# Kernel tuning notes

Hardware: AMD Instinct MI355X
Metric: run time of the kernel (lower is better)

Reference implementation:

```python
import jax, jax.numpy as jnp
import numpy as np
from jax import lax

RATE = 2
KSIZE = 3
FUSE_K = 3
SOFTMAX_SCALE = 10.0
EPS = 1e-8


def extract_patches(x, k, s):
    """ZeroPad2d(1) then unfold: x [B,C,H,W] -> patches [B, oh*ow, C, k, k]."""
    xp = jnp.pad(x, ((0, 0), (0, 0), (1, 1), (1, 1)))
    B, C, Hp, Wp = xp.shape
    oh = (Hp - k) // s + 1
    ow = (Wp - k) // s + 1
    ii = (jnp.arange(oh) * s)[:, None] + jnp.arange(k)[None, :]   # [oh,k]
    jj = (jnp.arange(ow) * s)[:, None] + jnp.arange(k)[None, :]   # [ow,k]
    p = xp[:, :, ii[:, :, None, None], jj[None, None, :, :]]      # [B,C,oh,k,ow,k]
    p = p.transpose(0, 2, 4, 1, 3, 5).reshape(B, oh * ow, C, k, k)
    return p


def _fuse_conv(a, eye):
    # a: [B,1,N,M]; 3x3 identity-diagonal smoothing conv, padding 1
    return lax.conv_general_dilated(a, eye, (1, 1), [(1, 1), (1, 1)],
                                    dimension_numbers=('NCHW', 'OIHW', 'NCHW'))


def contextual_attention(in_data, mask):
    B, C, H, W = in_data.shape
    Cf = C // 2
    f_full = in_data[:, :Cf]          # narrow(1,0,C//2)
    b_full = in_data[:, :Cf]          # source narrows the SAME slice for b
    mask_f = mask.astype(in_data.dtype)
    rate = RATE
    kernel = 2 * rate

    # raw 4x4 patches of full-res background (deconv filters), [B,L,Cf,4,4]
    raw_w = extract_patches(b_full, kernel, rate)

    # nearest downsample by 1/rate == strided slicing
    f = f_full[:, :, ::rate, ::rate]
    b = b_full[:, :, ::rate, ::rate]
    h, w = f.shape[2], f.shape[3]
    L = h * w

    # 3x3 matching patches of downsampled background, L2-normalized per patch
    wpat = extract_patches(b, KSIZE, 1)                              # [B,L,Cf,3,3]
    norm = jnp.sqrt(jnp.sum(wpat * wpat, axis=(2, 3, 4), keepdims=True))
    wn = wpat / jnp.maximum(norm, EPS)

    # per-sample conv2d(xi, wi_normed, padding=1) == patch/patch correlation
    fp = extract_patches(f, KSIZE, 1)                                # [B,hw,Cf,3,3]
    yi = jnp.einsum('bpckl,bqckl->bqp', fp, wn).reshape(B, L, h, w)  # [B,L,h,w]

    # fuse: two diagonal 3x3 smoothing passes over the [L, h*w] score matrix
    eye = jnp.eye(FUSE_K, dtype=in_data.dtype).reshape(1, 1, FUSE_K, FUSE_K)
    A = yi.reshape(B, 1, L, h * w)
    A = _fuse_conv(A, eye)
    A = A.reshape(B, h, w, h, w).transpose(0, 2, 1, 4, 3).reshape(B, 1, w * h, w * h)
    A = _fuse_conv(A, eye)
    A = A.reshape(B, w, h, w, h).transpose(0, 2, 1, 4, 3)
    yi = A.reshape(B, L, h, w)

    # mask gate: mm = 1 where the 3x3 mask patch is all-zero
    mpat = extract_patches(mask_f, KSIZE, 1)[0]                      # [L,1,3,3]
    m_mean = jnp.mean(mpat, axis=(1, 2, 3))                          # [L]
    mm = (m_mean == 0.0).astype(in_data.dtype)[None, :, None, None]
    yi = yi * mm
    yi = jax.nn.softmax(yi * SOFTMAX_SCALE, axis=1)
    yi = yi * mm

    # conv_transpose2d(yi, raw_wi, stride=rate, padding=1) / 4 per sample
    def agg(y1, rw):
        rhs = jnp.flip(rw, (-2, -1)).transpose(1, 0, 2, 3)           # [Cf,L,4,4]
        return lax.conv_general_dilated(y1[None], rhs, (1, 1), [(2, 2), (2, 2)],
                                        lhs_dilation=(rate, rate),
                                        dimension_numbers=('NCHW', 'OIHW', 'NCHW'))[0]
    y = jax.vmap(agg)(yi, raw_w) / 4.0                               # [B,Cf,H,W]

    # masked_fill_(inv_mask, 0) == multiply by {0,1} mask, upsampled to H x W
    mask_up = jnp.repeat(jnp.repeat(mask_f, rate, axis=2), rate, axis=3)
    y = y * mask_up

    return jnp.concatenate([b_full, f_full, y], axis=1)             # [B,3*Cf,H,W]


def setup_inputs() -> dict:
    key = jax.random.key(0)
    k1, k2 = jax.random.split(key)
    in_data = jax.random.normal(k1, (2, 128, 128, 128), dtype=jnp.float32)
    mask = jax.random.randint(k2, (1, 1, 64, 64), 0, 2, dtype=jnp.int32)
    return {"in_data": in_data, "mask": mask}


def reference(in_data, mask):
    return contextual_attention(in_data, mask)
```

## Files before the change

kernel.cpp:

```cpp
#include <hip/hip_runtime.h>
#include <math.h>

#define MAX_SLOTS 64
#define L 4096

#define OFF_CNT   0
#define OFF_LIST  64
#define OFF_FSUB  512
#define OFF_K5    2230784
#define OFF_SF    4065792

__device__ __forceinline__ void build_list(const int* __restrict__ mask,
                                           unsigned int* flagw, int* llist,
                                           int* lcnt) {
    int tid = threadIdx.x;
    for (int w = tid; w < 128; w += 256) flagw[w] = 0u;
    __syncthreads();
    int q0 = tid * 16;
    unsigned int mybits = 0u;
    for (int k = 0; k < 16; ++k) {
        int q = q0 + k;
        int qi = q >> 6, qj = q & 63;
        bool allz = true;
        for (int dy = -1; dy <= 1; ++dy)
            for (int dx = -1; dx <= 1; ++dx) {
                int y = qi + dy, x = qj + dx;
                if (y >= 0 && y < 64 && x >= 0 && x < 64)
                    allz = allz && (mask[y * 64 + x] == 0);
            }
        if (allz) mybits |= (1u << k);
    }
    if (mybits) atomicOr(&flagw[q0 >> 5], mybits << (q0 & 31));
    __syncthreads();
    if (tid < 64) {
        unsigned int w0 = flagw[2 * tid], w1 = flagw[2 * tid + 1];
        int own = __popc(w0) + __popc(w1);
        int inc = own;
        for (int o = 1; o < 64; o <<= 1) {
            int v = __shfl_up(inc, o);
            if (tid >= o) inc += v;
        }
        int pos = inc - own;
        for (int k = 0; k < 32; ++k)
            if (w0 & (1u << k)) { if (pos < MAX_SLOTS) llist[pos] = tid * 64 + k; ++pos; }
        for (int k = 0; k < 32; ++k)
            if (w1 & (1u << k)) { if (pos < MAX_SLOTS) llist[pos] = tid * 64 + 32 + k; ++pos; }
        if (tid == 63) *lcnt = (inc < MAX_SLOTS) ? inc : MAX_SLOTS;
    }
    __syncthreads();
}

__global__ __launch_bounds__(256) void k_front(const float* __restrict__ in,
                                               const int* __restrict__ mask,
                                               int* __restrict__ cnt,
                                               int* __restrict__ list,
                                               float* __restrict__ fsub,
                                               float* __restrict__ K5,
                                               float* __restrict__ sf,
                                               float* __restrict__ out) {
    __shared__ float patch9[5184];
    __shared__ unsigned int flagw[128];
    __shared__ int llist[MAX_SLOTS];
    __shared__ int lcnt;
    __shared__ int iflags[16];
    int tid = threadIdx.x;
    int blk = blockIdx.x;

    if (blk < 128) {
        int slot = blk & 63, b = blk >> 6;
        build_list(mask, flagw, llist, &lcnt);
        int nact = lcnt;
        if (blk == 0) {
            if (tid < MAX_SLOTS) list[tid] = llist[tid];
            if (tid == 64) *cnt = nact;
        }
        if (slot >= nact) {
            for (int t = tid; t < 1600; t += 256) {
                int c = t / 25, e = t - c * 25;
                K5[(((size_t)b * 64 + c) * 64 + slot) * 28 + e] = 0.f;
            }
            return;
        }
        if (tid < 16) iflags[tid] = 0;
        __syncthreads();
        int Q = llist[slot];
        const float* inb = in + (size_t)b * 2097152;
        int w = tid >> 6, lane = tid & 63;
        for (int combo = w; combo < 9; combo += 4) {
            int d2 = combo / 3 - 1, d1 = combo % 3 - 1;
            int XQ = ((Q & 63) << 6) + (Q >> 6) + d2;
            if (XQ < 0 || XQ >= L) continue;
            int YQ = ((XQ & 63) << 6) + (XQ >> 6);
            int R = YQ + d1;
            if (R < 0 || R >= L) continue;
            if (lane == 0) iflags[combo] = 1;
            int ri = R >> 6, rj = R & 63;
            float vals[9]; float ss = 0.f;
            #pragma unroll
            for (int k = 0; k < 9; ++k) {
                int t = lane + (k << 6);
                int c = t / 9; int tap = t - c * 9;
                int dy = tap / 3, dx = tap - dy * 3;
                int yy = ri + dy - 1, xx = rj + dx - 1;
                float v = ((unsigned)yy < 64u && (unsigned)xx < 64u)
                          ? inb[((size_t)c << 14) + (yy << 8) + (xx << 1)] : 0.f;
                vals[k] = v; ss += v * v;
            }
            for (int o = 32; o > 0; o >>= 1) ss += __shfl_xor(ss, o);
            float inv = 1.f / fmaxf(sqrtf(ss), 1e-8f);
            float* dst = patch9 + combo * 576;
            #pragma unroll
            for (int k = 0; k < 9; ++k) dst[lane + (k << 6)] = vals[k] * inv;
        }
        __syncthreads();
        for (int t = tid; t < 1600; t += 256) {
            int c = t / 25, e = t - c * 25;
            int oy = e / 5 - 2, ox = e - (e / 5) * 5 - 2;
            float s = 0.f;
            for (int dy = -1; dy <= 1; ++dy) {
                int dd2 = oy - dy; if (dd2 < -1 || dd2 > 1) continue;
                for (int dx = -1; dx <= 1; ++dx) {
                    int dd1 = ox - dx; if (dd1 < -1 || dd1 > 1) continue;
                    int combo = (dd2 + 1) * 3 + (dd1 + 1);
                    if (iflags[combo])
                        s += patch9[combo * 576 + c * 9 + (dy + 1) * 3 + (dx + 1)];
                }
            }
            K5[(((size_t)b * 64 + c) * 64 + slot) * 28 + e] = s;
        }
        return;
    }

    int idx = (blk - 128) * 256 + tid;
    int j = idx & 63;
    int i = (idx >> 6) & 63;
    int c = (idx >> 12) & 63;
    int b = idx >> 18;
    float v = in[(((b * 128 + c) * 128) + 2 * i) * 128 + 2 * j];
    fsub[(size_t)b * 278784 + c * 4356 + (i + 1) * 66 + (j + 1)] = v;
    sf[idx] = 0.f;
    if (idx < 33280) {
        int plane = idx / 260;
        int r = idx - plane * 260;
        int pb = plane >> 6, pc = plane & 63;
        int row, col;
        if (r < 66) { row = 0; col = r; }
        else if (r < 132) { row = 65; col = r - 66; }
        else { int rr = r - 132; row = (rr >> 1) + 1; col = (rr & 1) ? 65 : 0; }
        fsub[(size_t)pb * 278784 + pc * 4356 + row * 66 + col] = 0.f;
    }
    #pragma unroll
    for (int k = 0; k < 4; ++k) {
        int t = idx + k * 524288;
        int pix = t & 16383;
        int cc = (t >> 14) & 63;
        int bb = t >> 20;
        float pv = in[(size_t)(bb * 128 + cc) * 16384 + pix];
        size_t ob = (size_t)bb * 3145728;
        out[ob + (size_t)cc * 16384 + pix] = pv;
        out[ob + (size_t)(cc + 64) * 16384 + pix] = pv;
    }
}

__global__ __launch_bounds__(256) void k_mid2(const int* __restrict__ cnt,
                                              const int* __restrict__ list,
                                              const float* __restrict__ fsub,
                                              const float* __restrict__ K5,
                                              float* __restrict__ sf) {
    __shared__ float smem[840];
    int tid = threadIdx.x;
    int blk = blockIdx.x;
    int nact = min(*cnt, MAX_SLOTS);
    if (nact == 0) return;

    if (blk < 496) {
        int wid = __builtin_amdgcn_readfirstlane(blk * 4 + (tid >> 6));
        int j = tid & 63;
        int r   = 1 + (wid % 62);
        int cg2 = (wid / 62) & 15;
        int b   = wid / 992;
        int jc = min(max(j, 1), 62);
        const float* F = fsub + (size_t)b * 278784;
        int base = (r - 1) * 66 + (jc - 1);
        bool active = (j >= 1 && j <= 62);
        int P = (r << 6) + j;
        for (int s0 = 0; s0 < nact; s0 += 16) {
            float acc[16];
            #pragma unroll
            for (int s = 0; s < 16; ++s) acc[s] = 0.f;
            #pragma unroll
            for (int cc = 0; cc < 4; ++cc) {
                int c = cg2 * 4 + cc;
                const float* Fc = F + c * 4356 + base;
                float win[25];
                #pragma unroll
                for (int dy = 0; dy < 5; ++dy)
                    #pragma unroll
                    for (int dx = 0; dx < 5; ++dx)
                        win[dy * 5 + dx] = Fc[dy * 66 + dx];
                const float* kc = K5 + (((size_t)b * 64 + c) * 64 + s0) * 28;
                #pragma unroll
                for (int s = 0; s < 16; ++s) {
                    #pragma unroll
                    for (int k = 0; k < 25; ++k)
                        acc[s] += kc[s * 28 + k] * win[k];
                }
            }
            if (active) {
                int smax = min(16, nact - s0);
                for (int s = 0; s < smax; ++s)
                    atomicAdd(&sf[((size_t)b * 64 + (s0 + s)) * 4096 + P], acc[s]);
            }
        }
        return;
    }

    int bt = blk - 496;
    int combo = bt % 9; int rest = bt / 9;
    int slot = rest & 63, b = rest >> 6;
    if (slot >= nact) return;
    int d2 = combo / 3 - 1, d1 = combo % 3 - 1;
    int Q = list[slot];
    int XQ = ((Q & 63) << 6) + (Q >> 6) + d2;
    if (XQ < 0 || XQ >= L) return;
    int YQ = ((XQ & 63) << 6) + (XQ >> 6);
    int R = YQ + d1;
    if (R < 0 || R >= L) return;
    int ri = R >> 6, rj = R & 63;
    const float* F = fsub + (size_t)b * 278784;
    float* patch = smem;
    float* red = smem + 576;
    const float* Fp = F + ri * 66 + rj;
    auto ld = [&](int t) -> float {
        int c = t / 9; int tap = t - c * 9;
        int dy = tap / 3, dx = tap - dy * 3;
        return Fp[c * 4356 + dy * 66 + dx];
    };
    float v0 = ld(tid), v1 = ld(tid + 256), v2 = (tid < 64) ? ld(tid + 512) : 0.f;
    red[tid] = v0 * v0 + v1 * v1 + v2 * v2;
    __syncthreads();
    if (tid < 64) {
        float a = red[tid] + red[tid + 64] + red[tid + 128] + red[tid + 192];
        for (int o = 32; o > 0; o >>= 1) a += __shfl_xor(a, o);
        if (tid == 0) smem[832] = 1.f / fmaxf(sqrtf(a), 1e-8f);
    }
    __syncthreads();
    float inv = smem[832];
    patch[tid] = v0 * inv; patch[tid + 256] = v1 * inv;
    if (tid < 64) patch[tid + 512] = v2 * inv;
    __syncthreads();
    if (tid >= 252) return;
    int i, j;
    if (tid < 64)       { i = 0;  j = tid; }
    else if (tid < 128) { i = 63; j = tid - 64; }
    else if (tid < 190) { i = tid - 127; j = 0; }
    else                { i = tid - 189; j = 63; }
    int P = (i << 6) + j;
    int XP = (j << 6) + i + d2;
    if (XP < 0 || XP >= L) return;
    int YP = ((XP & 63) << 6) + (XP >> 6);
    int Z = YP + d1;
    if (Z < 0 || Z >= L) return;
    int pi = Z >> 6, pj = Z & 63;
    const float* Fz = F + pi * 66 + pj;
    float dot = 0.f;
    #pragma unroll 4
    for (int c = 0; c < 64; ++c) {
        const float* Fc = Fz + c * 4356;
        const float* pc = patch + c * 9;
        dot += Fc[0] * pc[0]   + Fc[1] * pc[1]   + Fc[2] * pc[2];
        dot += Fc[66] * pc[3]  + Fc[67] * pc[4]  + Fc[68] * pc[5];
        dot += Fc[132] * pc[6] + Fc[133] * pc[7] + Fc[134] * pc[8];
    }
    atomicAdd(&sf[((size_t)b * 64 + slot) * 4096 + P], dot);
}

__global__ __launch_bounds__(256) void k_tail2(const float* __restrict__ in,
                                               const int* __restrict__ mask,
                                               const int* __restrict__ cnt,
                                               const int* __restrict__ list,
                                               const float* __restrict__ sf,
                                               float* __restrict__ out) {
    __shared__ float sw16[16 * 192];
    __shared__ float pat16[16 * 128];
    __shared__ float Mv[192];
    __shared__ float Dv[192];
    int tid = threadIdx.x;
    int nact = min(*cnt, MAX_SLOTS);
    int up = blockIdx.x, cg8 = blockIdx.y, b = blockIdx.z;
    int c0 = cg8 * 8;
    const float* inb0 = in + (size_t)b * 2097152 + (size_t)c0 * 16384;
    const float* sfb = sf + (size_t)b * 262144;

    if (tid < 192) {
        int i = up - 1 + (tid >> 6); int jj = tid & 63;
        float M = 0.f, invden = 0.f;
        if ((unsigned)i < 64u && nact > 0) {
            const float* sp = sfb + (i << 6) + jj;
            for (int s = 0; s < nact; ++s)
                M = fmaxf(M, 10.f * sp[(size_t)s * 4096]);
            float den = (float)(L - nact) * expf(-M);
            for (int s = 0; s < nact; ++s)
                den += expf(10.f * sp[(size_t)s * 4096] - M);
            invden = 1.f / den;
        }
        Mv[tid] = M; Dv[tid] = invden;
    }

    int uu = tid >> 7, v = tid & 127;
    int u = up * 2 + uu;
    bool gate = (mask[(u >> 1) * 64 + (v >> 1)] != 0) && (nact > 0);
    int Wp[4]; int tap[4]; bool val[4];
    {
        int pa = (u + 1) & 1, pb_ = (v + 1) & 1;
        int i0 = (u + 1 - pa) >> 1, j0 = (v + 1 - pb_) >> 1;
        #pragma unroll
        for (int di = 0; di < 2; ++di)
            #pragma unroll
            for (int dj = 0; dj < 2; ++dj) {
                int p = di * 2 + dj;
                int ii = i0 - di, jx = j0 - dj;
                int iis = ii - (up - 1);
                val[p] = (jx >= 0 && jx < 64);
                Wp[p] = val[p] ? (iis * 64 + jx) : 0;
                tap[p] = (pa + 2 * di) * 4 + (pb_ + 2 * dj);
            }
    }
    float y[8];
    #pragma unroll
    for (int cc = 0; cc < 8; ++cc) y[cc] = 0.f;

    for (int s0 = 0; s0 < nact; s0 += 16) {
        int ns = min(16, nact - s0);
        __syncthreads();
        for (int t = tid; t < ns * 192; t += 256) {
            int sl = t / 192; int rr = t - sl * 192;
            int i = up - 1 + (rr >> 6); int jj = rr & 63;
            float wv = 0.f;
            if ((unsigned)i < 64u)
                wv = expf(10.f * sfb[(size_t)(s0 + sl) * 4096 + (i << 6) + jj] - Mv[rr]) * Dv[rr];
            sw16[t] = wv;
        }
        for (int t = tid; t < ns * 128; t += 256) {
            int sl = t >> 7; int rr = t & 127;
            int cc = rr >> 4; int e = rr & 15; int aa = e >> 2; int bb = e & 3;
            int q = list[s0 + sl]; int qi = q >> 6, qj = q & 63;
            int row = 2 * qi - 1 + aa, col = 2 * qj - 1 + bb;
            float pv = (row >= 0 && row < 128 && col >= 0 && col < 128)
                       ? inb0[(size_t)cc * 16384 + row * 128 + col] : 0.f;
            pat16[t] = pv;
        }
        __syncthreads();
        if (gate) {
            for (int s = 0; s < ns; ++s) {
                const float* wrow = sw16 + s * 192;
                const float* ps = pat16 + s * 128;
                #pragma unroll
                for (int p = 0; p < 4; ++p) {
                    if (!val[p]) continue;
                    float wv = wrow[Wp[p]];
                    #pragma unroll
                    for (int cc = 0; cc < 8; ++cc)
                        y[cc] += wv * ps[cc * 16 + tap[p]];
                }
            }
        }
    }
    if (gate) {
        #pragma unroll
        for (int cc = 0; cc < 8; ++cc) y[cc] *= 0.25f;
    }
    size_t ob = (size_t)b * 3145728 + (size_t)(c0 + 128) * 16384 + (size_t)u * 128 + v;
    #pragma unroll
    for (int cc = 0; cc < 8; ++cc)
        out[ob + (size_t)cc * 16384] = y[cc];
}

extern "C" void kernel_launch(void* const* d_in, const int* in_sizes, int n_in,
                              void* d_out, int out_size, void* d_ws, size_t ws_size,
                              hipStream_t stream) {
    const float* in = (const float*)d_in[0];
    const int* mask = (const int*)d_in[1];
    float* out = (float*)d_out;
    char* ws = (char*)d_ws;
    int* cnt    = (int*)(ws + OFF_CNT);
    int* list   = (int*)(ws + OFF_LIST);
    float* fsub = (float*)(ws + OFF_FSUB);
    float* K5   = (float*)(ws + OFF_K5);
    float* sf   = (float*)(ws + OFF_SF);

    k_front<<<2176, 256, 0, stream>>>(in, mask, cnt, list, fsub, K5, sf, out);
    k_mid2<<<1648, 256, 0, stream>>>(cnt, list, fsub, K5, sf);
    k_tail2<<<dim3(64, 8, 2), 256, 0, stream>>>(in, mask, cnt, list, sf, out);
}
```

Baseline: 146.0 us.

## Fuse three kernels into one persistent kernel with grid-wide barriers

Merges the front, mid and tail kernels into a single persistent kernel of 1024 blocks that loops over the old block indices and separates the phases with a software global barrier built on atomics. The aim is to remove two kernel launches and the gaps between them. It also vectorizes the copy to the output and the zeroing of sf with float4, and cuts the slot batch in the mid phase from 16 to 8 to save registers. In exchange it relies on all 1024 blocks being resident at once (launch bounds 256,4), pays for spin-wait barriers, and every phase now shares one pool of shared memory.

Measured after the change: 513.5 us. 3.52x slower.

```diff
diff --git a/kernel.cpp b/kernel.cpp
--- a/kernel.cpp
+++ b/kernel.cpp
@@ -3,12 +3,35 @@
 
 #define MAX_SLOTS 64
 #define L 4096
+#define NBLK 1024
 
 #define OFF_CNT   0
 #define OFF_LIST  64
 #define OFF_FSUB  512
 #define OFF_K5    2230784
 #define OFF_SF    4065792
+
+__device__ unsigned int g_bar[4];
+
+__device__ __forceinline__ void global_barrier(int which) {
+    __syncthreads();
+    if (threadIdx.x == 0) {
+        unsigned int* cntp = &g_bar[which * 2];
+        unsigned int* genp = &g_bar[which * 2 + 1];
+        __threadfence();
+        unsigned int g = __hip_atomic_load(genp, __ATOMIC_RELAXED, __HIP_MEMORY_SCOPE_AGENT);
+        unsigned int a = __hip_atomic_fetch_add(cntp, 1u, __ATOMIC_ACQ_REL, __HIP_MEMORY_SCOPE_AGENT);
+        if (a == gridDim.x - 1) {
+            __hip_atomic_store(cntp, 0u, __ATOMIC_RELAXED, __HIP_MEMORY_SCOPE_AGENT);
+            __hip_atomic_store(genp, g + 1u, __ATOMIC_RELEASE, __HIP_MEMORY_SCOPE_AGENT);
+        } else {
+            while (__hip_atomic_load(genp, __ATOMIC_RELAXED, __HIP_MEMORY_SCOPE_AGENT) == g)
+                __builtin_amdgcn_s_sleep(1);
+        }
+        __threadfence();
+    }
+    __syncthreads();
+}
 
 __device__ __forceinline__ void build_list(const int* __restrict__ mask,
                                            unsigned int* flagw, int* llist,
@@ -50,330 +73,335 @@
     __syncthreads();
 }
 
-__global__ __launch_bounds__(256) void k_front(const float* __restrict__ in,
-                                               const int* __restrict__ mask,
-                                               int* __restrict__ cnt,
-                                               int* __restrict__ list,
-                                               float* __restrict__ fsub,
-                                               float* __restrict__ K5,
-                                               float* __restrict__ sf,
-                                               float* __restrict__ out) {
-    __shared__ float patch9[5184];
+__global__ __launch_bounds__(256, 4) void k_all(const float* __restrict__ in,
+                                                const int* __restrict__ mask,
+                                                int* __restrict__ cnt,
+                                                int* __restrict__ list,
+                                                float* __restrict__ fsub,
+                                                float* __restrict__ K5,
+                                                float* __restrict__ sf,
+                                                float* __restrict__ out) {
+    __shared__ float pool[5504];
     __shared__ unsigned int flagw[128];
     __shared__ int llist[MAX_SLOTS];
     __shared__ int lcnt;
     __shared__ int iflags[16];
     int tid = threadIdx.x;
-    int blk = blockIdx.x;
-
-    if (blk < 128) {
-        int slot = blk & 63, b = blk >> 6;
-        build_list(mask, flagw, llist, &lcnt);
-        int nact = lcnt;
-        if (blk == 0) {
-            if (tid < MAX_SLOTS) list[tid] = llist[tid];
-            if (tid == 64) *cnt = nact;
-        }
-        if (slot >= nact) {
-            for (int t = tid; t < 1600; t += 256) {
-                int c = t / 25, e = t - c * 25;
-                K5[(((size_t)b * 64 + c) * 64 + slot) * 28 + e] = 0.f;
-            }
-            return;
-        }
-        if (tid < 16) iflags[tid] = 0;
+    int bid = blockIdx.x;
+
+    for (int tt = bid; tt < 2176; tt += NBLK) {
+        if (tt < 128) {
+            int slot = tt & 63, b = tt >> 6;
+            build_list(mask, flagw, llist, &lcnt);
+            int nact = lcnt;
+            if (tt == 0) {
+                if (tid < MAX_SLOTS) list[tid] = llist[tid];
+                if (tid == 64) *cnt = nact;
+            }
+            if (slot >= nact) {
+                for (int t = tid; t < 1600; t += 256) {
+                    int c = t / 25, e = t - c * 25;
+                    K5[(((size_t)b * 64 + c) * 64 + slot) * 28 + e] = 0.f;
+                }
+            } else {
+                float* patch9 = pool;
+                if (tid < 16) iflags[tid] = 0;
+                __syncthreads();
+                int Q = llist[slot];
+                const float* inb = in + (size_t)b * 2097152;
+                int w = tid >> 6, lane = tid & 63;
+                for (int combo = w; combo < 9; combo += 4) {
+                    int d2 = combo / 3 - 1, d1 = combo % 3 - 1;
+                    int XQ = ((Q & 63) << 6) + (Q >> 6) + d2;
+                    if (XQ < 0 || XQ >= L) continue;
+                    int YQ = ((XQ & 63) << 6) + (XQ >> 6);
+                    int R = YQ + d1;
+                    if (R < 0 || R >= L) continue;
+                    if (lane == 0) iflags[combo] = 1;
+                    int ri = R >> 6, rj = R & 63;
+                    float vals[9]; float ss = 0.f;
+                    #pragma unroll
+                    for (int k = 0; k < 9; ++k) {
+                        int t = lane + (k << 6);
+                        int c = t / 9; int tap = t - c * 9;
+                        int dy = tap / 3, dx = tap - dy * 3;
+                        int yy = ri + dy - 1, xx = rj + dx - 1;
+                        float v = ((unsigned)yy < 64u && (unsigned)xx < 64u)
+                                  ? inb[((size_t)c << 14) + (yy << 8) + (xx << 1)] : 0.f;
+                        vals[k] = v; ss += v * v;
+                    }
+                    for (int o = 32; o > 0; o >>= 1) ss += __shfl_xor(ss, o);
+                    float inv = 1.f / fmaxf(sqrtf(ss), 1e-8f);
+                    float* dst = patch9 + combo * 576;
+                    #pragma unroll
+                    for (int k = 0; k < 9; ++k) dst[lane + (k << 6)] = vals[k] * inv;
+                }
+                __syncthreads();
+                for (int t = tid; t < 1600; t += 256) {
+                    int c = t / 25, e = t - c * 25;
+                    int oy = e / 5 - 2, ox = e - (e / 5) * 5 - 2;
+                    float s = 0.f;
+                    for (int dy = -1; dy <= 1; ++dy) {
+                        int dd2 = oy - dy; if (dd2 < -1 || dd2 > 1) continue;
+                        for (int dx = -1; dx <= 1; ++dx) {
+                            int dd1 = ox - dx; if (dd1 < -1 || dd1 > 1) continue;
+                            int combo = (dd2 + 1) * 3 + (dd1 + 1);
+                            if (iflags[combo])
+                                s += patch9[combo * 576 + c * 9 + (dy + 1) * 3 + (dx + 1)];
+                        }
+                    }
+                    K5[(((size_t)b * 64 + c) * 64 + slot) * 28 + e] = s;
+                }
+            }
+        } else {
+            int idx = (tt - 128) * 256 + tid;
+            int j = idx & 63;
+            int i = (idx >> 6) & 63;
+            int c = (idx >> 12) & 63;
+            int b = idx >> 18;
+            float v = in[(((b * 128 + c) * 128) + 2 * i) * 128 + 2 * j];
+            fsub[(size_t)b * 278784 + c * 4356 + (i + 1) * 66 + (j + 1)] = v;
+            if (idx < 131072) {
+                ((float4*)sf)[idx] = make_float4(0.f, 0.f, 0.f, 0.f);
+            }
+            if (idx < 33280) {
+                int plane = idx / 260;
+                int r = idx - plane * 260;
+                int pb = plane >> 6, pc = plane & 63;
+                int row, col;
+                if (r < 66) { row = 0; col = r; }
+                else if (r < 132) { row = 65; col = r - 66; }
+                else { int rr = r - 132; row = (rr >> 1) + 1; col = (rr & 1) ? 65 : 0; }
+                fsub[(size_t)pb * 278784 + pc * 4356 + row * 66 + col] = 0.f;
+            }
+            {
+                int pix4 = idx & 4095;
+                int cc = (idx >> 12) & 63;
+                int bb = idx >> 18;
+                const float4* in4 = (const float4*)in;
+                float4* out4 = (float4*)out;
+                float4 pv = in4[(size_t)idx + (size_t)bb * 262144];
+                size_t ob4 = (size_t)bb * 786432 + (size_t)cc * 4096 + pix4;
+                out4[ob4] = pv;
+                out4[ob4 + 262144] = pv;
+            }
+        }
+    }
+
+    global_barrier(0);
+
+    int nact = min(*cnt, MAX_SLOTS);
+    if (nact > 0) {
+        for (int tt = bid; tt < 1648; tt += NBLK) {
+            if (tt < 496) {
+                int wid = __builtin_amdgcn_readfirstlane(tt * 4 + (tid >> 6));
+                int j = tid & 63;
+                int r   = 1 + (wid % 62);
+                int cg2 = (wid / 62) & 15;
+                int b   = wid / 992;
+                int jc = min(max(j, 1), 62);
+                const float* F = fsub + (size_t)b * 278784;
+                int base = (r - 1) * 66 + (jc - 1);
+                bool active = (j >= 1 && j <= 62);
+                int P = (r << 6) + j;
+                for (int s0 = 0; s0 < nact; s0 += 8) {
+                    float acc[8];
+                    #pragma unroll
+                    for (int s = 0; s < 8; ++s) acc[s] = 0.f;
+                    #pragma unroll
+                    for (int cc = 0; cc < 4; ++cc) {
+                        int c = cg2 * 4 + cc;
+                        const float* Fc = F + c * 4356 + base;
+                        float win[25];
+                        #pragma unroll
+                        for (int dy = 0; dy < 5; ++dy)
+                            #pragma unroll
+                            for (int dx = 0; dx < 5; ++dx)
+                                win[dy * 5 + dx] = Fc[dy * 66 + dx];
+                        const float* kc = K5 + (((size_t)b * 64 + c) * 64 + s0) * 28;
+                        #pragma unroll
+                        for (int s = 0; s < 8; ++s) {
+                            #pragma unroll
+                            for (int k = 0; k < 25; ++k)
+                                acc[s] += kc[s * 28 + k] * win[k];
+                        }
+                    }
+                    if (active) {
+                        int smax = min(8, nact - s0);
+                        for (int s = 0; s < smax; ++s)
+                            atomicAdd(&sf[((size_t)b * 64 + (s0 + s)) * 4096 + P], acc[s]);
+                    }
+                }
+            } else {
+                int bt = tt - 496;
+                int combo = bt % 9; int rest = bt / 9;
+                int slot = rest & 63, b = rest >> 6;
+                bool ok = (slot < nact);
+                int d2 = combo / 3 - 1, d1 = combo % 3 - 1;
+                int ri = 0, rj = 0;
+                if (ok) {
+                    int Q = list[slot];
+                    int XQ = ((Q & 63) << 6) + (Q >> 6) + d2;
+                    ok = (XQ >= 0 && XQ < L);
+                    if (ok) {
+                        int YQ = ((XQ & 63) << 6) + (XQ >> 6);
+                        int R = YQ + d1;
+                        ok = (R >= 0 && R < L);
+                        if (ok) { ri = R >> 6; rj = R & 63; }
+                    }
+                }
+                if (ok) {
+                    const float* F = fsub + (size_t)b * 278784;
+                    float* patch = pool;
+                    float* red = pool + 576;
+                    const float* Fp = F + ri * 66 + rj;
+                    auto ld = [&](int t) -> float {
+                        int c = t / 9; int tap = t - c * 9;
+                        int dy = tap / 3, dx = tap - dy * 3;
+                        return Fp[c * 4356 + dy * 66 + dx];
+                    };
+                    float v0 = ld(tid), v1 = ld(tid + 256), v2 = (tid < 64) ? ld(tid + 512) : 0.f;
+                    red[tid] = v0 * v0 + v1 * v1 + v2 * v2;
+                    __syncthreads();
+                    if (tid < 64) {
+                        float a = red[tid] + red[tid + 64] + red[tid + 128] + red[tid + 192];
+                        for (int o = 32; o > 0; o >>= 1) a += __shfl_xor(a, o);
+                        if (tid == 0) pool[832] = 1.f / fmaxf(sqrtf(a), 1e-8f);
+                    }
+                    __syncthreads();
+                    float inv = pool[832];
+                    patch[tid] = v0 * inv; patch[tid + 256] = v1 * inv;
+                    if (tid < 64) patch[tid + 512] = v2 * inv;
+                    __syncthreads();
+                    if (tid < 252) {
+                        int i, j;
+                        if (tid < 64)       { i = 0;  j = tid; }
+                        else if (tid < 128) { i = 63; j = tid - 64; }
+                        else if (tid < 190) { i = tid - 127; j = 0; }
+                        else                { i = tid - 189; j = 63; }
+                        int P = (i << 6) + j;
+                        int XP = (j << 6) + i + d2;
+                        if (XP >= 0 && XP < L) {
+                            int YP = ((XP & 63) << 6) + (XP >> 6);
+                            int Z = YP + d1;
+                            if (Z >= 0 && Z < L) {
+                                int pi = Z >> 6, pj = Z & 63;
+                                const float* Fz = F + pi * 66 + pj;
+                                float dot = 0.f;
+                                #pragma unroll 4
+                                for (int c = 0; c < 64; ++c) {
+                                    const float* Fc = Fz + c * 4356;
+                                    const float* pc = patch + c * 9;
+                                    dot += Fc[0] * pc[0]   + Fc[1] * pc[1]   + Fc[2] * pc[2];
+                                    dot += Fc[66] * pc[3]  + Fc[67] * pc[4]  + Fc[68] * pc[5];
+                                    dot += Fc[132] * pc[6] + Fc[133] * pc[7] + Fc[134] * pc[8];
+                                }
+                                atomicAdd(&sf[((size_t)b * 64 + slot) * 4096 + P], dot);
+                            }
+                        }
+                    }
+                    __syncthreads();
+                }
+            }
+        }
+    }
+
+    global_barrier(1);
+
+    float* sw16  = pool;
+    float* pat16 = pool + 3072;
+    float* Mv    = pool + 5120;
+    float* Dv    = pool + 5312;
+    for (int tt = bid; tt < 1024; tt += NBLK) {
+        int up = tt & 63, cg8 = (tt >> 6) & 7, b = tt >> 9;
+        int c0 = cg8 * 8;
+        const float* inb0 = in + (size_t)b * 2097152 + (size_t)c0 * 16384;
+        const float* sfb = sf + (size_t)b * 262144;
+
+        if (tid < 192) {
+            int i = up - 1 + (tid >> 6); int jj = tid & 63;
+            float M = 0.f, invden = 0.f;
+            if ((unsigned)i < 64u && nact > 0) {
+                const float* sp = sfb + (i << 6) + jj;
+                for (int s = 0; s < nact; ++s)
+                    M = fmaxf(M, 10.f * sp[(size_t)s * 4096]);
+                float den = (float)(L - nact) * expf(-M);
+                for (int s = 0; s < nact; ++s)
+                    den += expf(10.f * sp[(size_t)s * 4096] - M);
+                invden = 1.f / den;
+            }
+            Mv[tid] = M; Dv[tid] = invden;
+        }
+
+        int uu = tid >> 7, v = tid & 127;
+        int u = up * 2 + uu;
+        bool gate = (mask[(u >> 1) * 64 + (v >> 1)] != 0) && (nact > 0);
+        int Wp[4]; int tap[4]; bool val[4];
+        {
+            int pa = (u + 1) & 1, pb_ = (v + 1) & 1;
+            int i0 = (u + 1 - pa) >> 1, j0 = (v + 1 - pb_) >> 1;
+            #pragma unroll
+            for (int di = 0; di < 2; ++di)
+                #pragma unroll
+                for (int dj = 0; dj < 2; ++dj) {
+                    int p = di * 2 + dj;
+                    int ii = i0 - di, jx = j0 - dj;
+                    int iis = ii - (up - 1);
+                    val[p] = (jx >= 0 && jx < 64);
+                    Wp[p] = val[p] ? (iis * 64 + jx) : 0;
+                    tap[p] = (pa + 2 * di) * 4 + (pb_ + 2 * dj);
+                }
+        }
+        float y[8];
+        #pragma unroll
+        for (int cc = 0; cc < 8; ++cc) y[cc] = 0.f;
+
+        for (int s0 = 0; s0 < nact; s0 += 16) {
+            int ns = min(16, nact - s0);
+            __syncthreads();
+            for (int t = tid; t < ns * 192; t += 256) {
+                int sl = t / 192; int rr = t - sl * 192;
+                int i = up - 1 + (rr >> 6); int jj = rr & 63;
+                float wv = 0.f;
+                if ((unsigned)i < 64u)
+                    wv = expf(10.f * sfb[(size_t)(s0 + sl) * 4096 + (i << 6) + jj] - Mv[rr]) * Dv[rr];
+                sw16[t] = wv;
+            }
+            for (int t = tid; t < ns * 128; t += 256) {
+                int sl = t >> 7; int rr = t & 127;
+                int cc = rr >> 4; int e = rr & 15; int aa = e >> 2; int bb = e & 3;
+                int q = list[s0 + sl]; int qi = q >> 6, qj = q & 63;
+                int row = 2 * qi - 1 + aa, col = 2 * qj - 1 + bb;
+                float pv = (row >= 0 && row < 128 && col >= 0 && col < 128)
+                           ? inb0[(size_t)cc * 16384 + row * 128 + col] : 0.f;
+                pat16[t] = pv;
+            }
+            __syncthreads();
+            if (gate) {
+                for (int s = 0; s < ns; ++s) {
+                    const float* wrow = sw16 + s * 192;
+                    const float* ps = pat16 + s * 128;
+                    #pragma unroll
+                    for (int p = 0; p < 4; ++p) {
+                        if (!val[p]) continue;
+                        float wv = wrow[Wp[p]];
+                        #pragma unroll
+                        for (int cc = 0; cc < 8; ++cc)
+                            y[cc] += wv * ps[cc * 16 + tap[p]];
+                    }
+                }
+            }
+        }
+        if (gate) {
+            #pragma unroll
+            for (int cc = 0; cc < 8; ++cc) y[cc] *= 0.25f;
+        }
+        size_t ob = (size_t)b * 3145728 + (size_t)(c0 + 128) * 16384 + (size_t)u * 128 + v;
+        #pragma unroll
+        for (int cc = 0; cc < 8; ++cc)
+            out[ob + (size_t)cc * 16384] = y[cc];
         __syncthreads();
-        int Q = llist[slot];
-        const float* inb = in + (size_t)b * 2097152;
-        int w = tid >> 6, lane = tid & 63;
-        for (int combo = w; combo < 9; combo += 4) {
-            int d2 = combo / 3 - 1, d1 = combo % 3 - 1;
-            int XQ = ((Q & 63) << 6) + (Q >> 6) + d2;
-            if (XQ < 0 || XQ >= L) continue;
-            int YQ = ((XQ & 63) << 6) + (XQ >> 6);
-            int R = YQ + d1;
-            if (R < 0 || R >= L) continue;
-            if (lane == 0) iflags[combo] = 1;
-            int ri = R >> 6, rj = R & 63;
-            float vals[9]; float ss = 0.f;
-            #pragma unroll
-            for (int k = 0; k < 9; ++k) {
-                int t = lane + (k << 6);
-                int c = t / 9; int tap = t - c * 9;
-                int dy = tap / 3, dx = tap - dy * 3;
-                int yy = ri + dy - 1, xx = rj + dx - 1;
-                float v = ((unsigned)yy < 64u && (unsigned)xx < 64u)
-                          ? inb[((size_t)c << 14) + (yy << 8) + (xx << 1)] : 0.f;
-                vals[k] = v; ss += v * v;
-            }
-            for (int o = 32; o > 0; o >>= 1) ss += __shfl_xor(ss, o);
-            float inv = 1.f / fmaxf(sqrtf(ss), 1e-8f);
-            float* dst = patch9 + combo * 576;
-            #pragma unroll
-            for (int k = 0; k < 9; ++k) dst[lane + (k << 6)] = vals[k] * inv;
-        }
-        __syncthreads();
-        for (int t = tid; t < 1600; t += 256) {
-            int c = t / 25, e = t - c * 25;
-            int oy = e / 5 - 2, ox = e - (e / 5) * 5 - 2;
-            float s = 0.f;
-            for (int dy = -1; dy <= 1; ++dy) {
-                int dd2 = oy - dy; if (dd2 < -1 || dd2 > 1) continue;
-                for (int dx = -1; dx <= 1; ++dx) {
-                    int dd1 = ox - dx; if (dd1 < -1 || dd1 > 1) continue;
-                    int combo = (dd2 + 1) * 3 + (dd1 + 1);
-                    if (iflags[combo])
-                        s += patch9[combo * 576 + c * 9 + (dy + 1) * 3 + (dx + 1)];
-                }
-            }
-            K5[(((size_t)b * 64 + c) * 64 + slot) * 28 + e] = s;
-        }
-        return;
-    }
-
-    int idx = (blk - 128) * 256 + tid;
-    int j = idx & 63;
-    int i = (idx >> 6) & 63;
-    int c = (idx >> 12) & 63;
-    int b = idx >> 18;
-    float v = in[(((b * 128 + c) * 128) + 2 * i) * 128 + 2 * j];
-    fsub[(size_t)b * 278784 + c * 4356 + (i + 1) * 66 + (j + 1)] = v;
-    sf[idx] = 0.f;
-    if (idx < 33280) {
-        int plane = idx / 260;
-        int r = idx - plane * 260;
-        int pb = plane >> 6, pc = plane & 63;
-        int row, col;
-        if (r < 66) { row = 0; col = r; }
-        else if (r < 132) { row = 65; col = r - 66; }
-        else { int rr = r - 132; row = (rr >> 1) + 1; col = (rr & 1) ? 65 : 0; }
-        fsub[(size_t)pb * 278784 + pc * 4356 + row * 66 + col] = 0.f;
-    }
-    #pragma unroll
-    for (int k = 0; k < 4; ++k) {
-        int t = idx + k * 524288;
-        int pix = t & 16383;
-        int cc = (t >> 14) & 63;
-        int bb = t >> 20;
-        float pv = in[(size_t)(bb * 128 + cc) * 16384 + pix];
-        size_t ob = (size_t)bb * 3145728;
-        out[ob + (size_t)cc * 16384 + pix] = pv;
-        out[ob + (size_t)(cc + 64) * 16384 + pix] = pv;
-    }
-}
-
-__global__ __launch_bounds__(256) void k_mid2(const int* __restrict__ cnt,
-                                              const int* __restrict__ list,
-                                              const float* __restrict__ fsub,
-                                              const float* __restrict__ K5,
-                                              float* __restrict__ sf) {
-    __shared__ float smem[840];
-    int tid = threadIdx.x;
-    int blk = blockIdx.x;
-    int nact = min(*cnt, MAX_SLOTS);
-    if (nact == 0) return;
-
-    if (blk < 496) {
-        int wid = __builtin_amdgcn_readfirstlane(blk * 4 + (tid >> 6));
-        int j = tid & 63;
-        int r   = 1 + (wid % 62);
-        int cg2 = (wid / 62) & 15;
-        int b   = wid / 992;
-        int jc = min(max(j, 1), 62);
-        const float* F = fsub + (size_t)b * 278784;
-        int base = (r - 1) * 66 + (jc - 1);
-        bool active = (j >= 1 && j <= 62);
-        int P = (r << 6) + j;
-        for (int s0 = 0; s0 < nact; s0 += 16) {
-            float acc[16];
-            #pragma unroll
-            for (int s = 0; s < 16; ++s) acc[s] = 0.f;
-            #pragma unroll
-            for (int cc = 0; cc < 4; ++cc) {
-                int c = cg2 * 4 + cc;
-                const float* Fc = F + c * 4356 + base;
-                float win[25];
-                #pragma unroll
-                for (int dy = 0; dy < 5; ++dy)
-                    #pragma unroll
-                    for (int dx = 0; dx < 5; ++dx)
-                        win[dy * 5 + dx] = Fc[dy * 66 + dx];
-                const float* kc = K5 + (((size_t)b * 64 + c) * 64 + s0) * 28;
-                #pragma unroll
-                for (int s = 0; s < 16; ++s) {
-                    #pragma unroll
-                    for (int k = 0; k < 25; ++k)
-                        acc[s] += kc[s * 28 + k] * win[k];
-                }
-            }
-            if (active) {
-                int smax = min(16, nact - s0);
-                for (int s = 0; s < smax; ++s)
-                    atomicAdd(&sf[((size_t)b * 64 + (s0 + s)) * 4096 + P], acc[s]);
-            }
-        }
-        return;
-    }
-
-    int bt = blk - 496;
-    int combo = bt % 9; int rest = bt / 9;
-    int slot = rest & 63, b = rest >> 6;
-    if (slot >= nact) return;
-    int d2 = combo / 3 - 1, d1 = combo % 3 - 1;
-    int Q = list[slot];
-    int XQ = ((Q & 63) << 6) + (Q >> 6) + d2;
-    if (XQ < 0 || XQ >= L) return;
-    int YQ = ((XQ & 63) << 6) + (XQ >> 6);
-    int R = YQ + d1;
-    if (R < 0 || R >= L) return;
-    int ri = R >> 6, rj = R & 63;
-    const float* F = fsub + (size_t)b * 278784;
-    float* patch = smem;
-    float* red = smem + 576;
-    const float* Fp = F + ri * 66 + rj;
-    auto ld = [&](int t) -> float {
-        int c = t / 9; int tap = t - c * 9;
-        int dy = tap / 3, dx = tap - dy * 3;
-        return Fp[c * 4356 + dy * 66 + dx];
-    };
-    float v0 = ld(tid), v1 = ld(tid + 256), v2 = (tid < 64) ? ld(tid + 512) : 0.f;
-    red[tid] = v0 * v0 + v1 * v1 + v2 * v2;
-    __syncthreads();
-    if (tid < 64) {
-        float a = red[tid] + red[tid + 64] + red[tid + 128] + red[tid + 192];
-        for (int o = 32; o > 0; o >>= 1) a += __shfl_xor(a, o);
-        if (tid == 0) smem[832] = 1.f / fmaxf(sqrtf(a), 1e-8f);
-    }
-    __syncthreads();
-    float inv = smem[832];
-    patch[tid] = v0 * inv; patch[tid + 256] = v1 * inv;
-    if (tid < 64) patch[tid + 512] = v2 * inv;
-    __syncthreads();
-    if (tid >= 252) return;
-    int i, j;
-    if (tid < 64)       { i = 0;  j = tid; }
-    else if (tid < 128) { i = 63; j = tid - 64; }
-    else if (tid < 190) { i = tid - 127; j = 0; }
-    else                { i = tid - 189; j = 63; }
-    int P = (i << 6) + j;
-    int XP = (j << 6) + i + d2;
-    if (XP < 0 || XP >= L) return;
-    int YP = ((XP & 63) << 6) + (XP >> 6);
-    int Z = YP + d1;
-    if (Z < 0 || Z >= L) return;
-    int pi = Z >> 6, pj = Z & 63;
-    const float* Fz = F + pi * 66 + pj;
-    float dot = 0.f;
-    #pragma unroll 4
-    for (int c = 0; c < 64; ++c) {
-        const float* Fc = Fz + c * 4356;
-        const float* pc = patch + c * 9;
-        dot += Fc[0] * pc[0]   + Fc[1] * pc[1]   + Fc[2] * pc[2];
-        dot += Fc[66] * pc[3]  + Fc[67] * pc[4]  + Fc[68] * pc[5];
-        dot += Fc[132] * pc[6] + Fc[133] * pc[7] + Fc[134] * pc[8];
-    }
-    atomicAdd(&sf[((size_t)b * 64 + slot) * 4096 + P], dot);
-}
-
-__global__ __launch_bounds__(256) void k_tail2(const float* __restrict__ in,
-                                               const int* __restrict__ mask,
-                                               const int* __restrict__ cnt,
-                                               const int* __restrict__ list,
-                                               const float* __restrict__ sf,
-                                               float* __restrict__ out) {
-    __shared__ float sw16[16 * 192];
-    __shared__ float pat16[16 * 128];
-    __shared__ float Mv[192];
-    __shared__ float Dv[192];
-    int tid = threadIdx.x;
-    int nact = min(*cnt, MAX_SLOTS);
-    int up = blockIdx.x, cg8 = blockIdx.y, b = blockIdx.z;
-    int c0 = cg8 * 8;
-    const float* inb0 = in + (size_t)b * 2097152 + (size_t)c0 * 16384;
-    const float* sfb = sf + (size_t)b * 262144;
-
-    if (tid < 192) {
-        int i = up - 1 + (tid >> 6); int jj = tid & 63;
-        float M = 0.f, invden = 0.f;
-        if ((unsigned)i < 64u && nact > 0) {
-            const float* sp = sfb + (i << 6) + jj;
-            for (int s = 0; s < nact; ++s)
-                M = fmaxf(M, 10.f * sp[(size_t)s * 4096]);
-            float den = (float)(L - nact) * expf(-M);
-            for (int s = 0; s < nact; ++s)
-                den += expf(10.f * sp[(size_t)s * 4096] - M);
-            invden = 1.f / den;
-        }
-        Mv[tid] = M; Dv[tid] = invden;
-    }
-
-    int uu = tid >> 7, v = tid & 127;
-    int u = up * 2 + uu;
-    bool gate = (mask[(u >> 1) * 64 + (v >> 1)] != 0) && (nact > 0);
-    int Wp[4]; int tap[4]; bool val[4];
-    {
-        int pa = (u + 1) & 1, pb_ = (v + 1) & 1;
-        int i0 = (u + 1 - pa) >> 1, j0 = (v + 1 - pb_) >> 1;
-        #pragma unroll
-        for (int di = 0; di < 2; ++di)
-            #pragma unroll
-            for (int dj = 0; dj < 2; ++dj) {
-                int p = di * 2 + dj;
-                int ii = i0 - di, jx = j0 - dj;
-                int iis = ii - (up - 1);
-                val[p] = (jx >= 0 && jx < 64);
-                Wp[p] = val[p] ? (iis * 64 + jx) : 0;
-                tap[p] = (pa + 2 * di) * 4 + (pb_ + 2 * dj);
-            }
-    }
-    float y[8];
-    #pragma unroll
-    for (int cc = 0; cc < 8; ++cc) y[cc] = 0.f;
-
-    for (int s0 = 0; s0 < nact; s0 += 16) {
-        int ns = min(16, nact - s0);
-        __syncthreads();
-        for (int t = tid; t < ns * 192; t += 256) {
-            int sl = t / 192; int rr = t - sl * 192;
-            int i = up - 1 + (rr >> 6); int jj = rr & 63;
-            float wv = 0.f;
-            if ((unsigned)i < 64u)
-                wv = expf(10.f * sfb[(size_t)(s0 + sl) * 4096 + (i << 6) + jj] - Mv[rr]) * Dv[rr];
-            sw16[t] = wv;
-        }
-        for (int t = tid; t < ns * 128; t += 256) {
-            int sl = t >> 7; int rr = t & 127;
-            int cc = rr >> 4; int e = rr & 15; int aa = e >> 2; int bb = e & 3;
-            int q = list[s0 + sl]; int qi = q >> 6, qj = q & 63;
-            int row = 2 * qi - 1 + aa, col = 2 * qj - 1 + bb;
-            float pv = (row >= 0 && row < 128 && col >= 0 && col < 128)
-                       ? inb0[(size_t)cc * 16384 + row * 128 + col] : 0.f;
-            pat16[t] = pv;
-        }
-        __syncthreads();
-        if (gate) {
-            for (int s = 0; s < ns; ++s) {
-                const float* wrow = sw16 + s * 192;
-                const float* ps = pat16 + s * 128;
-                #pragma unroll
-                for (int p = 0; p < 4; ++p) {
-                    if (!val[p]) continue;
-                    float wv = wrow[Wp[p]];
-                    #pragma unroll
-                    for (int cc = 0; cc < 8; ++cc)
-                        y[cc] += wv * ps[cc * 16 + tap[p]];
-                }
-            }
-        }
-    }
-    if (gate) {
-        #pragma unroll
-        for (int cc = 0; cc < 8; ++cc) y[cc] *= 0.25f;
-    }
-    size_t ob = (size_t)b * 3145728 + (size_t)(c0 + 128) * 16384 + (size_t)u * 128 + v;
-    #pragma unroll
-    for (int cc = 0; cc < 8; ++cc)
-        out[ob + (size_t)cc * 16384] = y[cc];
+    }
 }
 
 extern "C" void kernel_launch(void* const* d_in, const int* in_sizes, int n_in,
@@ -389,7 +417,5 @@
     float* K5   = (float*)(ws + OFF_K5);
     float* sf   = (float*)(ws + OFF_SF);
 
-    k_front<<<2176, 256, 0, stream>>>(in, mask, cnt, list, fsub, K5, sf, out);
-    k_mid2<<<1648, 256, 0, stream>>>(cnt, list, fsub, K5, sf);
-    k_tail2<<<dim3(64, 8, 2), 256, 0, stream>>>(in, mask, cnt, list, sf, out);
+    k_all<<<NBLK, 256, 0, stream>>>(in, mask, cnt, list, fsub, K5, sf, out);
 }
```
